# Performance work log

Measured on AMD Instinct MI355X. Metric: run time of the kernel, lower is better.

Reference implementation:

```python
import jax, jax.numpy as jnp
import numpy as np

N_NODES = 100000
N_EDGES = 1000000
NODE_DIM = 128
LR_VOCAB = 2000
LR_EMBED = 32
HIDDEN = 128
IN_DIM = NODE_DIM * 4 + 1 + LR_EMBED  # 545


def setup_inputs() -> dict:
    key = jax.random.key(0)
    ks = jax.random.split(key, 10)
    z = jax.random.normal(ks[0], (N_NODES, NODE_DIM), dtype=jnp.float32)
    edge_index = jax.random.randint(ks[1], (2, N_EDGES), 0, N_NODES, dtype=jnp.int64)
    # edge_attr7: col 0 = dist (float in [0,1)), col 2 = lr_id (int-valued float in [0, LR_VOCAB))
    ea = jax.random.uniform(ks[2], (N_EDGES, 7), dtype=jnp.float32)
    lr_ids = jax.random.randint(ks[3], (N_EDGES,), 0, LR_VOCAB).astype(jnp.float32)
    edge_attr7 = ea.at[:, 2].set(lr_ids)
    lr_emb = jax.random.normal(ks[4], (LR_VOCAB, LR_EMBED), dtype=jnp.float32) * 0.02
    W1 = jax.random.normal(ks[5], (IN_DIM, HIDDEN), dtype=jnp.float32) * 0.02
    b1 = jnp.zeros((HIDDEN,), dtype=jnp.float32)
    W2 = jax.random.normal(ks[6], (HIDDEN, HIDDEN), dtype=jnp.float32) * 0.02
    b2 = jnp.zeros((HIDDEN,), dtype=jnp.float32)
    W3 = jax.random.normal(ks[7], (HIDDEN, 1), dtype=jnp.float32) * 0.02
    b3 = jnp.zeros((1,), dtype=jnp.float32)
    return {"z": z, "edge_index": edge_index, "edge_attr7": edge_attr7,
            "lr_emb": lr_emb, "W1": W1, "b1": b1, "W2": W2, "b2": b2,
            "W3": W3, "b3": b3}


def reference(z, edge_index, edge_attr7, lr_emb, W1, b1, W2, b2, W3, b3):
    src = edge_index[0]
    dst = edge_index[1]
    zs = z[src]                      # [E, D]
    zd = z[dst]                      # [E, D]
    dist = edge_attr7[:, 0:1]        # [E, 1]
    lr_id = edge_attr7[:, 2].astype(jnp.int32)
    lr_vec = lr_emb[lr_id]           # [E, LR_EMBED]
    x = jnp.concatenate([zs, zd, zs * zd, jnp.abs(zs - zd), dist, lr_vec], axis=1)  # [E, IN_DIM]
    h = jax.nn.relu(x @ W1 + b1)     # dropout is identity at inference
    h = jax.nn.relu(h @ W2 + b2)
    logit = (h @ W3 + b3).reshape(-1)  # [E]
    return logit
```

## Files before the change

kernel.cpp:

```cpp
#include <hip/hip_runtime.h>

#define N_EDGES 1000000
#define HID 128
#define ME 64

typedef unsigned short ushort;
typedef unsigned int uint;
typedef __attribute__((ext_vector_type(8))) short short8;
typedef __attribute__((ext_vector_type(4))) float f32x4;

__device__ __forceinline__ float blo(uint u) { return __builtin_bit_cast(float, u << 16); }
__device__ __forceinline__ float bhi(uint u) { return __builtin_bit_cast(float, u & 0xffff0000u); }
__device__ __forceinline__ ushort f2bfbits(float f) {
  uint u = __builtin_bit_cast(uint, f);
  return (ushort)((u + 0x7fffu + ((u >> 16) & 1u)) >> 16);
}
__device__ __forceinline__ uint cvtpk(float a, float b) {
  uint r;
  asm("v_cvt_pk_bf16_f32 %0, %1, %2" : "=v"(r) : "v"(a), "v"(b));
  return r;
}
__device__ __forceinline__ int sidx(int r, int c) {
  return r * 128 + (c ^ ((r & 7) << 3));
}

__global__ void prep_kernel(const float* __restrict__ W1, const float* __restrict__ W2,
                            ushort* __restrict__ W1p, ushort* __restrict__ W2p) {
  const int t = blockIdx.x * blockDim.x + threadIdx.x;
  const int n1 = 18 * 8 * 64 * 8;
  if (t < n1) {
    const int j = t & 7, lane = (t >> 3) & 63, nt = (t >> 9) & 7, kb = t >> 12;
    const int col = nt * 16 + (lane & 15);
    float val = 0.f;
    if (kb < 16) {
      const int k = kb * 32 + (lane >> 4) * 8 + j;
      val = W1[k * HID + col];
    } else {
      const int c = (kb - 16) * 32 + (lane >> 4) * 8 + j;
      const int k = (c == 0) ? 512 : ((c >= 2 && c < 34) ? (511 + c) : -1);
      if (k >= 0) val = W1[k * HID + col];
    }
    W1p[t] = f2bfbits(val);
  } else {
    const int t2 = t - n1;
    if (t2 < 4 * 8 * 64 * 8) {
      const int j = t2 & 7, lane = (t2 >> 3) & 63, nt = (t2 >> 9) & 7, kb = t2 >> 12;
      const int k = kb * 32 + (lane >> 4) * 8 + j;
      const int col = nt * 16 + (lane & 15);
      W2p[t2] = f2bfbits(W2[k * HID + col]);
    }
  }
}

__global__ __launch_bounds__(256, 3)
void edge_mlp(const float* __restrict__ z, const int* __restrict__ ei,
              const float* __restrict__ ea, const float* __restrict__ lre,
              const ushort* __restrict__ W1p, const float* __restrict__ b1,
              const ushort* __restrict__ W2p, const float* __restrict__ b2,
              const float* __restrict__ W3, const float* __restrict__ b3,
              float* __restrict__ out) {
  __shared__ ushort B0[ME * 128];
  __shared__ ushort B1[ME * 128];

  const int tid = threadIdx.x;
  const int lane = tid & 63;
  const int w = tid >> 6;
  const int r15 = lane & 15;
  const int g = lane >> 4;
  const int half = lane >> 5;
  const int li = lane & 31;
  const int row0 = w * 16;
  const int cw = w * 32;
  const int eb = blockIdx.x * ME;

  int sd = 0;
  float auxv = 0.f;
  if (lane < 16)      sd = ei[eb + row0 + lane];
  else if (lane < 32) sd = ei[N_EDGES + eb + row0 + (lane - 16)];
  else if (lane < 48) auxv = ea[(eb + row0 + (lane - 32)) * 7 + 0];
  else                auxv = ea[(eb + row0 + (lane - 48)) * 7 + 2];

  uint2 zs_pk[8], zd_pk[8];
#pragma unroll
  for (int t = 0; t < 8; ++t) {
    const int s = __shfl(sd, 2 * t + half);
    const float4 v = *(const float4*)(z + s * HID + 4 * li);
    zs_pk[t].x = cvtpk(v.x, v.y);
    zs_pk[t].y = cvtpk(v.z, v.w);
  }
#pragma unroll
  for (int t = 0; t < 8; ++t) {
    const int d = __shfl(sd, 16 + 2 * t + half);
    const float4 v = *(const float4*)(z + d * HID + 4 * li);
    zd_pk[t].x = cvtpk(v.x, v.y);
    zd_pk[t].y = cvtpk(v.z, v.w);
  }
#pragma unroll
  for (int t = 0; t < 8; ++t) {
    const int r = row0 + 2 * t + half;
    *(uint2*)&B0[sidx(r, 4 * li)] = zs_pk[t];
    *(uint2*)&B1[sidx(r, 4 * li)] = zd_pk[t];
  }
  __syncthreads();

  f32x4 acc[4][2];
#pragma unroll
  for (int mt = 0; mt < 4; ++mt) {
    acc[mt][0] = (f32x4){0.f, 0.f, 0.f, 0.f};
    acc[mt][1] = (f32x4){0.f, 0.f, 0.f, 0.f};
  }

#define MFMA_CHUNK(BUF, NKK, KB)                                                        \
  __builtin_amdgcn_s_setprio(1);                                                        \
  _Pragma("unroll")                                                                     \
  for (int kk = 0; kk < (NKK); ++kk) {                                                  \
    const int kbg = (KB) + kk;                                                          \
    short8 bfr0 = *(const short8*)(W1p + (((kbg * 8 + 2 * w) * 64) + lane) * 8);        \
    short8 bfr1 = *(const short8*)(W1p + (((kbg * 8 + 2 * w + 1) * 64) + lane) * 8);    \
    _Pragma("unroll")                                                                   \
    for (int mt = 0; mt < 4; ++mt) {                                                    \
      short8 af = *(const short8*)&BUF[sidx(mt * 16 + r15, kk * 32 + g * 8)];           \
      acc[mt][0] = __builtin_amdgcn_mfma_f32_16x16x32_bf16(af, bfr0, acc[mt][0], 0, 0, 0); \
      acc[mt][1] = __builtin_amdgcn_mfma_f32_16x16x32_bf16(af, bfr1, acc[mt][1], 0, 0, 0); \
    }                                                                                   \
  }                                                                                     \
  __builtin_amdgcn_s_setprio(0);

  MFMA_CHUNK(B0, 4, 0)
  __syncthreads();

#pragma unroll
  for (int t = 0; t < 8; ++t) {
    const int r = row0 + 2 * t + half;
    uint2 o;
    o.x = cvtpk(blo(zs_pk[t].x) * blo(zd_pk[t].x), bhi(zs_pk[t].x) * bhi(zd_pk[t].x));
    o.y = cvtpk(blo(zs_pk[t].y) * blo(zd_pk[t].y), bhi(zs_pk[t].y) * bhi(zd_pk[t].y));
    *(uint2*)&B0[sidx(r, 4 * li)] = o;
  }
  MFMA_CHUNK(B1, 4, 4)
  __syncthreads();

#pragma unroll
  for (int t = 0; t < 8; ++t) {
    const int r = row0 + 2 * t + half;
    uint2 o;
    o.x = cvtpk(fabsf(blo(zs_pk[t].x) - blo(zd_pk[t].x)),
                fabsf(bhi(zs_pk[t].x) - bhi(zd_pk[t].x)));
    o.y = cvtpk(fabsf(blo(zs_pk[t].y) - blo(zd_pk[t].y)),
                fabsf(bhi(zs_pk[t].y) - bhi(zd_pk[t].y)));
    *(uint2*)&B1[sidx(r, 4 * li)] = o;
  }
  MFMA_CHUNK(B0, 4, 8)
  __syncthreads();

  {
    const float dv = __shfl(auxv, 32 + r15);
    if (lane < 16) B0[sidx(row0 + lane, 0)] = f2bfbits(dv);
  }
#pragma unroll
  for (int t = 0; t < 4; ++t) {
    const int e = 4 * t + g;
    const int lrid = (int)__shfl(auxv, 48 + e);
    const float2 lv = *(const float2*)(lre + lrid * 32 + 2 * r15);
    *(uint*)&B0[sidx(row0 + e, 2 + 2 * r15)] = cvtpk(lv.x, lv.y);
  }
  MFMA_CHUNK(B1, 4, 12)
  __syncthreads();

  MFMA_CHUNK(B0, 2, 16)
  {
    const float b1v0 = b1[cw + r15];
    const float b1v1 = b1[cw + 16 + r15];
#pragma unroll
    for (int mt = 0; mt < 4; ++mt)
#pragma unroll
      for (int nt = 0; nt < 2; ++nt)
#pragma unroll
        for (int j = 0; j < 4; ++j) {
          const float h = acc[mt][nt][j] + (nt ? b1v1 : b1v0);
          B1[sidx(mt * 16 + g * 4 + j, cw + nt * 16 + r15)] = f2bfbits(fmaxf(h, 0.f));
        }
  }
  __syncthreads();

  f32x4 acc2[4][2];
#pragma unroll
  for (int mt = 0; mt < 4; ++mt) {
    acc2[mt][0] = (f32x4){0.f, 0.f, 0.f, 0.f};
    acc2[mt][1] = (f32x4){0.f, 0.f, 0.f, 0.f};
  }
  __builtin_amdgcn_s_setprio(1);
#pragma unroll
  for (int kk = 0; kk < 4; ++kk) {
    short8 bfr0 = *(const short8*)(W2p + (((kk * 8 + 2 * w) * 64) + lane) * 8);
    short8 bfr1 = *(const short8*)(W2p + (((kk * 8 + 2 * w + 1) * 64) + lane) * 8);
#pragma unroll
    for (int mt = 0; mt < 4; ++mt) {
      short8 af = *(const short8*)&B1[sidx(mt * 16 + r15, kk * 32 + g * 8)];
      acc2[mt][0] = __builtin_amdgcn_mfma_f32_16x16x32_bf16(af, bfr0, acc2[mt][0], 0, 0, 0);
      acc2[mt][1] = __builtin_amdgcn_mfma_f32_16x16x32_bf16(af, bfr1, acc2[mt][1], 0, 0, 0);
    }
  }
  __builtin_amdgcn_s_setprio(0);
  {
    const float b2v0 = b2[cw + r15];
    const float b2v1 = b2[cw + 16 + r15];
#pragma unroll
    for (int mt = 0; mt < 4; ++mt)
#pragma unroll
      for (int nt = 0; nt < 2; ++nt)
#pragma unroll
        for (int j = 0; j < 4; ++j) {
          const float h = acc2[mt][nt][j] + (nt ? b2v1 : b2v0);
          B0[sidx(mt * 16 + g * 4 + j, cw + nt * 16 + r15)] = f2bfbits(fmaxf(h, 0.f));
        }
  }
  __syncthreads();

  {
    const int rr = w * 16 + r15;
    float sum = 0.f;
#pragma unroll
    for (int i = 0; i < 4; ++i) {
      const int c0 = g * 32 + i * 8;
      const uint4 hv = *(const uint4*)&B0[sidx(rr, c0)];
#pragma unroll
      for (int p = 0; p < 4; ++p) {
        const uint u = ((const uint*)&hv)[p];
        const float2 wv = *(const float2*)(W3 + c0 + 2 * p);
        sum += blo(u) * wv.x + bhi(u) * wv.y;
      }
    }
    sum += __shfl_xor(sum, 16);
    sum += __shfl_xor(sum, 32);
    if (lane < 16) out[eb + rr] = sum + b3[0];
  }
}

extern "C" void kernel_launch(void* const* d_in, const int* in_sizes, int n_in,
                              void* d_out, int out_size, void* d_ws, size_t ws_size,
                              hipStream_t stream) {
  const float* z   = (const float*)d_in[0];
  const int*   ei  = (const int*)d_in[1];
  const float* ea  = (const float*)d_in[2];
  const float* lre = (const float*)d_in[3];
  const float* W1  = (const float*)d_in[4];
  const float* b1  = (const float*)d_in[5];
  const float* W2  = (const float*)d_in[6];
  const float* b2  = (const float*)d_in[7];
  const float* W3  = (const float*)d_in[8];
  const float* b3  = (const float*)d_in[9];
  float* out = (float*)d_out;

  ushort* W1p = (ushort*)d_ws;
  ushort* W2p = W1p + 18 * 8 * 64 * 8;

  prep_kernel<<<352, 256, 0, stream>>>(W1, W2, W1p, W2p);
  edge_mlp<<<N_EDGES / ME, 256, 0, stream>>>(z, ei, ea, lre, W1p, b1, W2p, b2, W3, b3, out);
}
```

Measured before the change: 290.3 us.

## Make each wave own its 16 edge rows and drop block barriers

Each wave now computes all 128 hidden columns for its own 16 edges instead of splitting columns across waves. Its LDS rows are therefore private, and every __syncthreads between the layer stages is removed. The elementwise product and abs-difference features are computed from the fp32 gathers and packed early with an abs-modifier conversion, rather than being rebuilt from bf16 values. In exchange, each wave loads the full W1 and W2 fragments, roughly quadrupling weight traffic per block through the caches, and it holds more accumulator registers.

New measurement: 563.0 us. 1.94x slower.

```diff
diff --git a/kernel.cpp b/kernel.cpp
--- a/kernel.cpp
+++ b/kernel.cpp
@@ -18,6 +18,11 @@
 __device__ __forceinline__ uint cvtpk(float a, float b) {
   uint r;
   asm("v_cvt_pk_bf16_f32 %0, %1, %2" : "=v"(r) : "v"(a), "v"(b));
+  return r;
+}
+__device__ __forceinline__ uint cvtpk_abs(float a, float b) {
+  uint r;
+  asm("v_cvt_pk_bf16_f32 %0, abs(%1), abs(%2)" : "=v"(r) : "v"(a), "v"(b));
   return r;
 }
 __device__ __forceinline__ int sidx(int r, int c) {
@@ -70,7 +75,6 @@
   const int half = lane >> 5;
   const int li = lane & 31;
   const int row0 = w * 16;
-  const int cw = w * 32;
   const int eb = blockIdx.x * ME;
 
   int sd = 0;
@@ -80,150 +84,115 @@
   else if (lane < 48) auxv = ea[(eb + row0 + (lane - 32)) * 7 + 0];
   else                auxv = ea[(eb + row0 + (lane - 48)) * 7 + 2];
 
-  uint2 zs_pk[8], zd_pk[8];
+  uint2 pr_pk[8], ad_pk[8];
 #pragma unroll
   for (int t = 0; t < 8; ++t) {
-    const int s = __shfl(sd, 2 * t + half);
-    const float4 v = *(const float4*)(z + s * HID + 4 * li);
-    zs_pk[t].x = cvtpk(v.x, v.y);
-    zs_pk[t].y = cvtpk(v.z, v.w);
-  }
-#pragma unroll
-  for (int t = 0; t < 8; ++t) {
-    const int d = __shfl(sd, 16 + 2 * t + half);
-    const float4 v = *(const float4*)(z + d * HID + 4 * li);
-    zd_pk[t].x = cvtpk(v.x, v.y);
-    zd_pk[t].y = cvtpk(v.z, v.w);
-  }
-#pragma unroll
-  for (int t = 0; t < 8; ++t) {
-    const int r = row0 + 2 * t + half;
-    *(uint2*)&B0[sidx(r, 4 * li)] = zs_pk[t];
-    *(uint2*)&B1[sidx(r, 4 * li)] = zd_pk[t];
-  }
-  __syncthreads();
-
-  f32x4 acc[4][2];
-#pragma unroll
-  for (int mt = 0; mt < 4; ++mt) {
-    acc[mt][0] = (f32x4){0.f, 0.f, 0.f, 0.f};
-    acc[mt][1] = (f32x4){0.f, 0.f, 0.f, 0.f};
-  }
-
-#define MFMA_CHUNK(BUF, NKK, KB)                                                        \
-  __builtin_amdgcn_s_setprio(1);                                                        \
-  _Pragma("unroll")                                                                     \
-  for (int kk = 0; kk < (NKK); ++kk) {                                                  \
-    const int kbg = (KB) + kk;                                                          \
-    short8 bfr0 = *(const short8*)(W1p + (((kbg * 8 + 2 * w) * 64) + lane) * 8);        \
-    short8 bfr1 = *(const short8*)(W1p + (((kbg * 8 + 2 * w + 1) * 64) + lane) * 8);    \
+    const int e = 2 * t + half;
+    const int r = row0 + e;
+    const int s = __shfl(sd, e);
+    const int d = __shfl(sd, 16 + e);
+    const float4 a = *(const float4*)(z + s * HID + 4 * li);
+    const float4 b = *(const float4*)(z + d * HID + 4 * li);
+    uint2 zs, zd;
+    zs.x = cvtpk(a.x, a.y); zs.y = cvtpk(a.z, a.w);
+    zd.x = cvtpk(b.x, b.y); zd.y = cvtpk(b.z, b.w);
+    *(uint2*)&B0[sidx(r, 4 * li)] = zs;
+    *(uint2*)&B1[sidx(r, 4 * li)] = zd;
+    pr_pk[t].x = cvtpk(a.x * b.x, a.y * b.y);
+    pr_pk[t].y = cvtpk(a.z * b.z, a.w * b.w);
+    ad_pk[t].x = cvtpk_abs(a.x - b.x, a.y - b.y);
+    ad_pk[t].y = cvtpk_abs(a.z - b.z, a.w - b.w);
+  }
+
+  f32x4 acc1[8];
+#pragma unroll
+  for (int nt = 0; nt < 8; ++nt) acc1[nt] = (f32x4){0.f, 0.f, 0.f, 0.f};
+
+#define MFMA_KB(BUF, WP, KBG, ACC)                                                      \
+  {                                                                                     \
+    const int kk_ = (KBG) & 3;                                                          \
+    short8 af = *(const short8*)&BUF[sidx(row0 + r15, kk_ * 32 + g * 8)];               \
     _Pragma("unroll")                                                                   \
-    for (int mt = 0; mt < 4; ++mt) {                                                    \
-      short8 af = *(const short8*)&BUF[sidx(mt * 16 + r15, kk * 32 + g * 8)];           \
-      acc[mt][0] = __builtin_amdgcn_mfma_f32_16x16x32_bf16(af, bfr0, acc[mt][0], 0, 0, 0); \
-      acc[mt][1] = __builtin_amdgcn_mfma_f32_16x16x32_bf16(af, bfr1, acc[mt][1], 0, 0, 0); \
+    for (int nt = 0; nt < 8; ++nt) {                                                    \
+      short8 bfr = *(const short8*)(WP + ((((KBG) * 8 + nt) * 64) + lane) * 8);         \
+      ACC[nt] = __builtin_amdgcn_mfma_f32_16x16x32_bf16(af, bfr, ACC[nt], 0, 0, 0);     \
     }                                                                                   \
-  }                                                                                     \
-  __builtin_amdgcn_s_setprio(0);
-
-  MFMA_CHUNK(B0, 4, 0)
-  __syncthreads();
-
-#pragma unroll
-  for (int t = 0; t < 8; ++t) {
-    const int r = row0 + 2 * t + half;
-    uint2 o;
-    o.x = cvtpk(blo(zs_pk[t].x) * blo(zd_pk[t].x), bhi(zs_pk[t].x) * bhi(zd_pk[t].x));
-    o.y = cvtpk(blo(zs_pk[t].y) * blo(zd_pk[t].y), bhi(zs_pk[t].y) * bhi(zd_pk[t].y));
-    *(uint2*)&B0[sidx(r, 4 * li)] = o;
-  }
-  MFMA_CHUNK(B1, 4, 4)
-  __syncthreads();
-
-#pragma unroll
-  for (int t = 0; t < 8; ++t) {
-    const int r = row0 + 2 * t + half;
-    uint2 o;
-    o.x = cvtpk(fabsf(blo(zs_pk[t].x) - blo(zd_pk[t].x)),
-                fabsf(bhi(zs_pk[t].x) - bhi(zd_pk[t].x)));
-    o.y = cvtpk(fabsf(blo(zs_pk[t].y) - blo(zd_pk[t].y)),
-                fabsf(bhi(zs_pk[t].y) - bhi(zd_pk[t].y)));
-    *(uint2*)&B1[sidx(r, 4 * li)] = o;
-  }
-  MFMA_CHUNK(B0, 4, 8)
-  __syncthreads();
+  }
+
+  __builtin_amdgcn_s_setprio(1);
+#pragma unroll
+  for (int kb = 0; kb < 4; ++kb) MFMA_KB(B0, W1p, kb, acc1)
+  __builtin_amdgcn_s_setprio(0);
+#pragma unroll
+  for (int t = 0; t < 8; ++t)
+    *(uint2*)&B0[sidx(row0 + 2 * t + half, 4 * li)] = pr_pk[t];
+
+  __builtin_amdgcn_s_setprio(1);
+#pragma unroll
+  for (int kb = 4; kb < 8; ++kb) MFMA_KB(B1, W1p, kb, acc1)
+  __builtin_amdgcn_s_setprio(0);
+#pragma unroll
+  for (int t = 0; t < 8; ++t)
+    *(uint2*)&B1[sidx(row0 + 2 * t + half, 4 * li)] = ad_pk[t];
+
+  __builtin_amdgcn_s_setprio(1);
+#pragma unroll
+  for (int kb = 8; kb < 12; ++kb) MFMA_KB(B0, W1p, kb, acc1)
+
+#pragma unroll
+  for (int kb = 12; kb < 16; ++kb) MFMA_KB(B1, W1p, kb, acc1)
+  __builtin_amdgcn_s_setprio(0);
 
   {
     const float dv = __shfl(auxv, 32 + r15);
-    if (lane < 16) B0[sidx(row0 + lane, 0)] = f2bfbits(dv);
+    if (lane < 16) B1[sidx(row0 + lane, 0)] = f2bfbits(dv);
   }
 #pragma unroll
   for (int t = 0; t < 4; ++t) {
     const int e = 4 * t + g;
     const int lrid = (int)__shfl(auxv, 48 + e);
     const float2 lv = *(const float2*)(lre + lrid * 32 + 2 * r15);
-    *(uint*)&B0[sidx(row0 + e, 2 + 2 * r15)] = cvtpk(lv.x, lv.y);
-  }
-  MFMA_CHUNK(B1, 4, 12)
-  __syncthreads();
-
-  MFMA_CHUNK(B0, 2, 16)
+    *(uint*)&B1[sidx(row0 + e, 2 + 2 * r15)] = cvtpk(lv.x, lv.y);
+  }
+  __builtin_amdgcn_s_setprio(1);
+#pragma unroll
+  for (int kb = 16; kb < 18; ++kb) MFMA_KB(B1, W1p, kb, acc1)
+  __builtin_amdgcn_s_setprio(0);
+
+#pragma unroll
+  for (int nt = 0; nt < 8; ++nt) {
+    const float bv = b1[nt * 16 + r15];
+#pragma unroll
+    for (int j = 0; j < 4; ++j) {
+      const float h = acc1[nt][j] + bv;
+      B0[sidx(row0 + g * 4 + j, nt * 16 + r15)] = f2bfbits(fmaxf(h, 0.f));
+    }
+  }
+
+  f32x4 acc2[8];
+#pragma unroll
+  for (int nt = 0; nt < 8; ++nt) acc2[nt] = (f32x4){0.f, 0.f, 0.f, 0.f};
+  __builtin_amdgcn_s_setprio(1);
+#pragma unroll
+  for (int kb = 0; kb < 4; ++kb) MFMA_KB(B0, W2p, kb, acc2)
+  __builtin_amdgcn_s_setprio(0);
+
+#pragma unroll
+  for (int nt = 0; nt < 8; ++nt) {
+    const float bv = b2[nt * 16 + r15];
+#pragma unroll
+    for (int j = 0; j < 4; ++j) {
+      const float h = acc2[nt][j] + bv;
+      B1[sidx(row0 + g * 4 + j, nt * 16 + r15)] = f2bfbits(fmaxf(h, 0.f));
+    }
+  }
+
   {
-    const float b1v0 = b1[cw + r15];
-    const float b1v1 = b1[cw + 16 + r15];
-#pragma unroll
-    for (int mt = 0; mt < 4; ++mt)
-#pragma unroll
-      for (int nt = 0; nt < 2; ++nt)
-#pragma unroll
-        for (int j = 0; j < 4; ++j) {
-          const float h = acc[mt][nt][j] + (nt ? b1v1 : b1v0);
-          B1[sidx(mt * 16 + g * 4 + j, cw + nt * 16 + r15)] = f2bfbits(fmaxf(h, 0.f));
-        }
-  }
-  __syncthreads();
-
-  f32x4 acc2[4][2];
-#pragma unroll
-  for (int mt = 0; mt < 4; ++mt) {
-    acc2[mt][0] = (f32x4){0.f, 0.f, 0.f, 0.f};
-    acc2[mt][1] = (f32x4){0.f, 0.f, 0.f, 0.f};
-  }
-  __builtin_amdgcn_s_setprio(1);
-#pragma unroll
-  for (int kk = 0; kk < 4; ++kk) {
-    short8 bfr0 = *(const short8*)(W2p + (((kk * 8 + 2 * w) * 64) + lane) * 8);
-    short8 bfr1 = *(const short8*)(W2p + (((kk * 8 + 2 * w + 1) * 64) + lane) * 8);
-#pragma unroll
-    for (int mt = 0; mt < 4; ++mt) {
-      short8 af = *(const short8*)&B1[sidx(mt * 16 + r15, kk * 32 + g * 8)];
-      acc2[mt][0] = __builtin_amdgcn_mfma_f32_16x16x32_bf16(af, bfr0, acc2[mt][0], 0, 0, 0);
-      acc2[mt][1] = __builtin_amdgcn_mfma_f32_16x16x32_bf16(af, bfr1, acc2[mt][1], 0, 0, 0);
-    }
-  }
-  __builtin_amdgcn_s_setprio(0);
-  {
-    const float b2v0 = b2[cw + r15];
-    const float b2v1 = b2[cw + 16 + r15];
-#pragma unroll
-    for (int mt = 0; mt < 4; ++mt)
-#pragma unroll
-      for (int nt = 0; nt < 2; ++nt)
-#pragma unroll
-        for (int j = 0; j < 4; ++j) {
-          const float h = acc2[mt][nt][j] + (nt ? b2v1 : b2v0);
-          B0[sidx(mt * 16 + g * 4 + j, cw + nt * 16 + r15)] = f2bfbits(fmaxf(h, 0.f));
-        }
-  }
-  __syncthreads();
-
-  {
-    const int rr = w * 16 + r15;
     float sum = 0.f;
 #pragma unroll
     for (int i = 0; i < 4; ++i) {
       const int c0 = g * 32 + i * 8;
-      const uint4 hv = *(const uint4*)&B0[sidx(rr, c0)];
+      const uint4 hv = *(const uint4*)&B1[sidx(row0 + r15, c0)];
 #pragma unroll
       for (int p = 0; p < 4; ++p) {
         const uint u = ((const uint*)&hv)[p];
@@ -233,7 +202,7 @@
     }
     sum += __shfl_xor(sum, 16);
     sum += __shfl_xor(sum, 32);
-    if (lane < 16) out[eb + rr] = sum + b3[0];
+    if (lane < 16) out[eb + row0 + r15] = sum + b3[0];
   }
 }
 
```

## Add third LDS buffer, compute features once in fp32, and cut barriers

Applied to the files above, without the earlier changes.

Adds a third shared buffer so zs, zd and zs*zd are all written up front, with the product and |zs-zd| computed from fp32 inputs rather than bf16-unpacked values. The first three K-chunks of the layer-1 GEMM then run back to back with only one barrier, and the abs term is folded into the packed convert via an abs modifier. This removes several __syncthreads and the repacking ALU work between MFMA chunks. In exchange LDS per block grows by half, which may lower occupancy below the launch-bounds target of 3 blocks, and the product now rounds from fp32 instead of bf16 operands.

Measured after the change: 328.8 us. 1.13x slower.

```diff
diff --git a/kernel.cpp b/kernel.cpp
--- a/kernel.cpp
+++ b/kernel.cpp
@@ -18,6 +18,11 @@
 __device__ __forceinline__ uint cvtpk(float a, float b) {
   uint r;
   asm("v_cvt_pk_bf16_f32 %0, %1, %2" : "=v"(r) : "v"(a), "v"(b));
+  return r;
+}
+__device__ __forceinline__ uint cvtpk_abs(float a, float b) {
+  uint r;
+  asm("v_cvt_pk_bf16_f32 %0, abs(%1), abs(%2)" : "=v"(r) : "v"(a), "v"(b));
   return r;
 }
 __device__ __forceinline__ int sidx(int r, int c) {
@@ -61,6 +66,7 @@
               float* __restrict__ out) {
   __shared__ ushort B0[ME * 128];
   __shared__ ushort B1[ME * 128];
+  __shared__ ushort B2[ME * 128];
 
   const int tid = threadIdx.x;
   const int lane = tid & 63;
@@ -80,26 +86,25 @@
   else if (lane < 48) auxv = ea[(eb + row0 + (lane - 32)) * 7 + 0];
   else                auxv = ea[(eb + row0 + (lane - 48)) * 7 + 2];
 
-  uint2 zs_pk[8], zd_pk[8];
+  uint2 ad_pk[8];
 #pragma unroll
   for (int t = 0; t < 8; ++t) {
-    const int s = __shfl(sd, 2 * t + half);
-    const float4 v = *(const float4*)(z + s * HID + 4 * li);
-    zs_pk[t].x = cvtpk(v.x, v.y);
-    zs_pk[t].y = cvtpk(v.z, v.w);
-  }
-#pragma unroll
-  for (int t = 0; t < 8; ++t) {
-    const int d = __shfl(sd, 16 + 2 * t + half);
-    const float4 v = *(const float4*)(z + d * HID + 4 * li);
-    zd_pk[t].x = cvtpk(v.x, v.y);
-    zd_pk[t].y = cvtpk(v.z, v.w);
-  }
-#pragma unroll
-  for (int t = 0; t < 8; ++t) {
-    const int r = row0 + 2 * t + half;
-    *(uint2*)&B0[sidx(r, 4 * li)] = zs_pk[t];
-    *(uint2*)&B1[sidx(r, 4 * li)] = zd_pk[t];
+    const int e = 2 * t + half;
+    const int r = row0 + e;
+    const int s = __shfl(sd, e);
+    const int d = __shfl(sd, 16 + e);
+    const float4 a = *(const float4*)(z + s * HID + 4 * li);
+    const float4 b = *(const float4*)(z + d * HID + 4 * li);
+    uint2 zs, zd, pr;
+    zs.x = cvtpk(a.x, a.y); zs.y = cvtpk(a.z, a.w);
+    zd.x = cvtpk(b.x, b.y); zd.y = cvtpk(b.z, b.w);
+    pr.x = cvtpk(a.x * b.x, a.y * b.y);
+    pr.y = cvtpk(a.z * b.z, a.w * b.w);
+    *(uint2*)&B0[sidx(r, 4 * li)] = zs;
+    *(uint2*)&B1[sidx(r, 4 * li)] = zd;
+    *(uint2*)&B2[sidx(r, 4 * li)] = pr;
+    ad_pk[t].x = cvtpk_abs(a.x - b.x, a.y - b.y);
+    ad_pk[t].y = cvtpk_abs(a.z - b.z, a.w - b.w);
   }
   __syncthreads();
 
@@ -111,7 +116,6 @@
   }
 
 #define MFMA_CHUNK(BUF, NKK, KB)                                                        \
-  __builtin_amdgcn_s_setprio(1);                                                        \
   _Pragma("unroll")                                                                     \
   for (int kk = 0; kk < (NKK); ++kk) {                                                  \
     const int kbg = (KB) + kk;                                                          \
@@ -119,55 +123,39 @@
     short8 bfr1 = *(const short8*)(W1p + (((kbg * 8 + 2 * w + 1) * 64) + lane) * 8);    \
     _Pragma("unroll")                                                                   \
     for (int mt = 0; mt < 4; ++mt) {                                                    \
-      short8 af = *(const short8*)&BUF[sidx(mt * 16 + r15, kk * 32 + g * 8)];           \
+      short8 af = *(const short8*)&BUF[sidx(mt * 16 + r15, ((kbg) & 3) * 32 + g * 8)];  \
       acc[mt][0] = __builtin_amdgcn_mfma_f32_16x16x32_bf16(af, bfr0, acc[mt][0], 0, 0, 0); \
       acc[mt][1] = __builtin_amdgcn_mfma_f32_16x16x32_bf16(af, bfr1, acc[mt][1], 0, 0, 0); \
     }                                                                                   \
-  }                                                                                     \
+  }
+
+  __builtin_amdgcn_s_setprio(1);
+  MFMA_CHUNK(B0, 4, 0)
+  MFMA_CHUNK(B1, 4, 4)
+  MFMA_CHUNK(B2, 4, 8)
   __builtin_amdgcn_s_setprio(0);
-
-  MFMA_CHUNK(B0, 4, 0)
-  __syncthreads();
-
-#pragma unroll
-  for (int t = 0; t < 8; ++t) {
-    const int r = row0 + 2 * t + half;
-    uint2 o;
-    o.x = cvtpk(blo(zs_pk[t].x) * blo(zd_pk[t].x), bhi(zs_pk[t].x) * bhi(zd_pk[t].x));
-    o.y = cvtpk(blo(zs_pk[t].y) * blo(zd_pk[t].y), bhi(zs_pk[t].y) * bhi(zd_pk[t].y));
-    *(uint2*)&B0[sidx(r, 4 * li)] = o;
-  }
-  MFMA_CHUNK(B1, 4, 4)
-  __syncthreads();
-
-#pragma unroll
-  for (int t = 0; t < 8; ++t) {
-    const int r = row0 + 2 * t + half;
-    uint2 o;
-    o.x = cvtpk(fabsf(blo(zs_pk[t].x) - blo(zd_pk[t].x)),
-                fabsf(bhi(zs_pk[t].x) - bhi(zd_pk[t].x)));
-    o.y = cvtpk(fabsf(blo(zs_pk[t].y) - blo(zd_pk[t].y)),
-                fabsf(bhi(zs_pk[t].y) - bhi(zd_pk[t].y)));
-    *(uint2*)&B1[sidx(r, 4 * li)] = o;
-  }
-  MFMA_CHUNK(B0, 4, 8)
-  __syncthreads();
-
+  __syncthreads();
+
+#pragma unroll
+  for (int t = 0; t < 8; ++t)
+    *(uint2*)&B0[sidx(row0 + 2 * t + half, 4 * li)] = ad_pk[t];
   {
     const float dv = __shfl(auxv, 32 + r15);
-    if (lane < 16) B0[sidx(row0 + lane, 0)] = f2bfbits(dv);
+    if (lane < 16) B1[sidx(row0 + lane, 0)] = f2bfbits(dv);
   }
 #pragma unroll
   for (int t = 0; t < 4; ++t) {
     const int e = 4 * t + g;
     const int lrid = (int)__shfl(auxv, 48 + e);
     const float2 lv = *(const float2*)(lre + lrid * 32 + 2 * r15);
-    *(uint*)&B0[sidx(row0 + e, 2 + 2 * r15)] = cvtpk(lv.x, lv.y);
-  }
-  MFMA_CHUNK(B1, 4, 12)
-  __syncthreads();
-
-  MFMA_CHUNK(B0, 2, 16)
+    *(uint*)&B1[sidx(row0 + e, 2 + 2 * r15)] = cvtpk(lv.x, lv.y);
+  }
+  __syncthreads();
+
+  __builtin_amdgcn_s_setprio(1);
+  MFMA_CHUNK(B0, 4, 12)
+  MFMA_CHUNK(B1, 2, 16)
+  __builtin_amdgcn_s_setprio(0);
   {
     const float b1v0 = b1[cw + r15];
     const float b1v1 = b1[cw + 16 + r15];
@@ -178,7 +166,7 @@
 #pragma unroll
         for (int j = 0; j < 4; ++j) {
           const float h = acc[mt][nt][j] + (nt ? b1v1 : b1v0);
-          B1[sidx(mt * 16 + g * 4 + j, cw + nt * 16 + r15)] = f2bfbits(fmaxf(h, 0.f));
+          B2[sidx(mt * 16 + g * 4 + j, cw + nt * 16 + r15)] = f2bfbits(fmaxf(h, 0.f));
         }
   }
   __syncthreads();
@@ -196,7 +184,7 @@
     short8 bfr1 = *(const short8*)(W2p + (((kk * 8 + 2 * w + 1) * 64) + lane) * 8);
 #pragma unroll
     for (int mt = 0; mt < 4; ++mt) {
-      short8 af = *(const short8*)&B1[sidx(mt * 16 + r15, kk * 32 + g * 8)];
+      short8 af = *(const short8*)&B2[sidx(mt * 16 + r15, kk * 32 + g * 8)];
       acc2[mt][0] = __builtin_amdgcn_mfma_f32_16x16x32_bf16(af, bfr0, acc2[mt][0], 0, 0, 0);
       acc2[mt][1] = __builtin_amdgcn_mfma_f32_16x16x32_bf16(af, bfr1, acc2[mt][1], 0, 0, 0);
     }
```
